# Optimization experiments

Measured on AMD Instinct MI355X. Metric: run time of the kernel, lower is better.

Reference implementation:

```python
import jax, jax.numpy as jnp
import numpy as np

BN_EPS = 1e-5
TAU = 1.0  # gumbel temperature

def setup_inputs() -> dict:
    key = jax.random.key(0)
    ks = jax.random.split(key, 6)
    B, O, F, H, HID = 32, 4096, 256, 8, 128
    x = jax.random.normal(ks[0], (B, O, F), dtype=jnp.float32)
    gumbel_noise = jax.random.gumbel(ks[1], (B, O, H), dtype=jnp.float32)
    W_in = jax.random.normal(ks[2], (F, HID), dtype=jnp.float32) * (1.0 / np.sqrt(F))
    b_in = jnp.zeros((HID,), jnp.float32)
    W_blk = jax.random.normal(ks[3], (HID, HID), dtype=jnp.float32) * (1.0 / np.sqrt(HID))
    b_blk = jnp.zeros((HID,), jnp.float32)
    bn_gamma = jnp.ones((HID,), jnp.float32)
    bn_beta = jnp.zeros((HID,), jnp.float32)
    W_fc = jax.random.normal(ks[4], (HID, H), dtype=jnp.float32) * (1.0 / np.sqrt(HID))
    b_fc = jnp.zeros((H,), jnp.float32)
    return {"x": x, "gumbel_noise": gumbel_noise, "W_in": W_in, "b_in": b_in,
            "W_blk": W_blk, "b_blk": b_blk, "bn_gamma": bn_gamma, "bn_beta": bn_beta,
            "W_fc": W_fc, "b_fc": b_fc}

def reference(x, gumbel_noise, W_in, b_in, W_blk, b_blk, bn_gamma, bn_beta, W_fc, b_fc):
    B, O, F = x.shape
    xf = x.reshape(B * O, F)
    # DynamicNetwork head: input linear + relu, one residual block (Linear+BN+ReLU), fc
    h = jax.nn.relu(xf @ W_in + b_in)  # (B*O, HID)
    z = h @ W_blk + b_blk
    mu = z.mean(axis=0)
    var = z.var(axis=0)  # biased var, matches BatchNorm training normalization
    z = (z - mu) * jax.lax.rsqrt(var + BN_EPS) * bn_gamma + bn_beta
    h = jax.nn.relu(z) + h  # residual
    logits = (h @ W_fc + b_fc).reshape(B, O, -1)  # (B, O, H)
    # mask out zero-norm observations
    mask = (jnp.linalg.norm(x, axis=2) != 0)[..., None].astype(x.dtype)  # (B, O, 1)
    logits = logits * mask
    # gumbel softmax over observation dim (soft)
    w = jax.nn.softmax((logits + gumbel_noise) / TAU, axis=1)  # (B, O, H)
    # weighted sum pooling: algebraically the repeat-multiply-sum in the original
    pooled = jnp.einsum('boh,bof->bhf', w, x)  # (B, H, F)
    return pooled.reshape(B, -1)  # (B, H*F)
```

## Files before the change

### kernel.cpp

```cpp
#include <hip/hip_runtime.h>
#include <hip/hip_bf16.h>
#include <math.h>

#define MB_ 131072
#define F_  256
#define HID_ 128
#define H_  8
#define O_  4096
#define B_  32

typedef __attribute__((ext_vector_type(8))) short short8;
typedef __attribute__((ext_vector_type(4))) float f32x4;

static __device__ __forceinline__ unsigned short f2bf(float f) {
    unsigned int u = __float_as_uint(f);
    unsigned int r = (u + 0x7fffu + ((u >> 16) & 1u)) >> 16;
    return (unsigned short)r;
}
static __device__ __forceinline__ float bf2f(unsigned short u) {
    return __uint_as_float(((unsigned int)u) << 16);
}
static __device__ __forceinline__ unsigned int pk2bf(float a, float b) {
    float2 f2; f2.x = a; f2.y = b;
    __hip_bfloat162 h = __float22bfloat162_rn(f2);
    union { __hip_bfloat162 h2; unsigned int u; } cv;
    cv.h2 = h;
    return cv.u;
}

__global__ __launch_bounds__(256) void k_prep(
    const float* __restrict__ W_in, const float* __restrict__ W_blk,
    unsigned short* __restrict__ Win_f, unsigned short* __restrict__ Wblk_f)
{
    const int idx = blockIdx.x * 256 + threadIdx.x;
    if (idx < 32768) {
        const int j = idx & 7, n = (idx >> 3) & 127, c = idx >> 10;
        Win_f[idx] = f2bf(W_in[(size_t)(c * 8 + j) * HID_ + n]);
    } else if (idx < 49152) {
        const int i2 = idx - 32768;
        const int j = i2 & 7, n = (i2 >> 3) & 127, c = i2 >> 10;
        Wblk_f[i2] = f2bf(W_blk[(size_t)(c * 8 + j) * HID_ + n]);
    }
}

__global__ __launch_bounds__(256, 3) void k_phaseA(
    const float* __restrict__ x, const unsigned short* __restrict__ Win_f,
    const unsigned short* __restrict__ Wblk_f,
    const float* __restrict__ b_in, const float* __restrict__ b_blk,
    unsigned short* __restrict__ h_out, float* __restrict__ mask_out,
    float* __restrict__ sumP, float* __restrict__ sumsqP)
{
    __shared__ __align__(16) unsigned short a_s[2][4 * 132 * 8];
    __shared__ __align__(16) unsigned short hb_s[128 * 136];
    __shared__ float csum_s[128], csumsq_s[128];

    const int tid = threadIdx.x;
    const int R0 = blockIdx.x * 128;
    const int wave = tid >> 6;
    const int wrow = wave >> 1, wcol = wave & 1;
    const int lane = tid & 63;
    const int lm = lane & 15, quad = lane >> 4;
    const int srow = tid >> 3;
    const int sk = tid & 7;
    const int sq = sk >> 1, sh = sk & 1;

    if (tid < 128) { csum_s[tid] = 0.f; csumsq_s[tid] = 0.f; }

    f32x4 acc[4][4];
#pragma unroll
    for (int i = 0; i < 4; i++)
#pragma unroll
        for (int j = 0; j < 4; j++) acc[i][j] = (f32x4){0.f, 0.f, 0.f, 0.f};
    float ms[4] = {0.f, 0.f, 0.f, 0.f};

    const float* xrow = x + (size_t)(R0 + srow) * F_ + sk * 4;

#pragma unroll
    for (int p = 0; p < 4; p++) {
        const float4 v = *(const float4*)(xrow + (size_t)(32 * p) * F_);
        ms[p] += v.x * v.x + v.y * v.y + v.z * v.z + v.w * v.w;
        uint2 w; w.x = pk2bf(v.x, v.y); w.y = pk2bf(v.z, v.w);
        *(uint2*)(&a_s[0][(sq * 132 + srow + 32 * p) * 8 + sh * 4]) = w;
    }
    __syncthreads();

    for (int kt = 0; kt < 8; kt++) {
        const int cur = kt & 1;
        float4 nv[4];
        if (kt < 7) {
#pragma unroll
            for (int p = 0; p < 4; p++)
                nv[p] = *(const float4*)(xrow + (kt + 1) * 32 + (size_t)(32 * p) * F_);
        }
        short8 bfr[4], af[4];
        const unsigned short* wf = Win_f + ((size_t)(kt * 4 + quad) * 128 + wcol * 64 + lm) * 8;
#pragma unroll
        for (int ni = 0; ni < 4; ni++)
            bfr[ni] = *(const short8*)(wf + ni * 16 * 8);
#pragma unroll
        for (int mi = 0; mi < 4; mi++)
            af[mi] = *(const short8*)(&a_s[cur][(quad * 132 + wrow * 64 + mi * 16 + lm) * 8]);
#pragma unroll
        for (int mi = 0; mi < 4; mi++)
#pragma unroll
            for (int ni = 0; ni < 4; ni++)
                acc[mi][ni] = __builtin_amdgcn_mfma_f32_16x16x32_bf16(af[mi], bfr[ni], acc[mi][ni], 0, 0, 0);
        if (kt < 7) {
#pragma unroll
            for (int p = 0; p < 4; p++) {
                ms[p] += nv[p].x * nv[p].x + nv[p].y * nv[p].y
                       + nv[p].z * nv[p].z + nv[p].w * nv[p].w;
                uint2 w; w.x = pk2bf(nv[p].x, nv[p].y); w.y = pk2bf(nv[p].z, nv[p].w);
                *(uint2*)(&a_s[1 - cur][(sq * 132 + srow + 32 * p) * 8 + sh * 4]) = w;
            }
        }
        __syncthreads();
    }

#pragma unroll
    for (int p = 0; p < 4; p++) {
        float s = ms[p];
        s += __shfl_down(s, 4, 8);
        s += __shfl_down(s, 2, 8);
        s += __shfl_down(s, 1, 8);
        if (sk == 0) mask_out[R0 + srow + 32 * p] = (s != 0.f) ? 1.f : 0.f;
    }

    {
        float bcol[4];
#pragma unroll
        for (int ni = 0; ni < 4; ni++) bcol[ni] = b_in[wcol * 64 + ni * 16 + lm];
#pragma unroll
        for (int mi = 0; mi < 4; mi++)
#pragma unroll
            for (int r = 0; r < 4; r++) {
                const int row = wrow * 64 + mi * 16 + quad * 4 + r;
#pragma unroll
                for (int ni = 0; ni < 4; ni++) {
                    const int col = wcol * 64 + ni * 16 + lm;
                    hb_s[row * 136 + col] = f2bf(fmaxf(acc[mi][ni][r] + bcol[ni], 0.f));
                }
            }
    }
    __syncthreads();

    {
        const int row = tid >> 1, half = tid & 1;
#pragma unroll
        for (int c8 = 0; c8 < 8; c8++) {
            const short8 v = *(const short8*)(&hb_s[row * 136 + half * 64 + c8 * 8]);
            *(short8*)(h_out + (size_t)(R0 + row) * HID_ + half * 64 + c8 * 8) = v;
        }
    }

#pragma unroll
    for (int i = 0; i < 4; i++)
#pragma unroll
        for (int j = 0; j < 4; j++) acc[i][j] = (f32x4){0.f, 0.f, 0.f, 0.f};
#pragma unroll
    for (int kt = 0; kt < 4; kt++) {
        short8 af[4], bfr[4];
        const unsigned short* wf2 = Wblk_f + ((size_t)(kt * 4 + quad) * 128 + wcol * 64 + lm) * 8;
#pragma unroll
        for (int ni = 0; ni < 4; ni++)
            bfr[ni] = *(const short8*)(wf2 + ni * 16 * 8);
#pragma unroll
        for (int mi = 0; mi < 4; mi++)
            af[mi] = *(const short8*)(&hb_s[(wrow * 64 + mi * 16 + lm) * 136 + kt * 32 + quad * 8]);
#pragma unroll
        for (int mi = 0; mi < 4; mi++)
#pragma unroll
            for (int ni = 0; ni < 4; ni++)
                acc[mi][ni] = __builtin_amdgcn_mfma_f32_16x16x32_bf16(af[mi], bfr[ni], acc[mi][ni], 0, 0, 0);
    }

    {
        float bcol[4];
#pragma unroll
        for (int ni = 0; ni < 4; ni++) bcol[ni] = b_blk[wcol * 64 + ni * 16 + lm];
        float s_c[4] = {0.f, 0.f, 0.f, 0.f}, ss_c[4] = {0.f, 0.f, 0.f, 0.f};
#pragma unroll
        for (int mi = 0; mi < 4; mi++)
#pragma unroll
            for (int r = 0; r < 4; r++)
#pragma unroll
                for (int ni = 0; ni < 4; ni++) {
                    const float zv = acc[mi][ni][r] + bcol[ni];
                    s_c[ni] += zv;
                    ss_c[ni] += zv * zv;
                }
#pragma unroll
        for (int ni = 0; ni < 4; ni++) {
            float s = s_c[ni], ss = ss_c[ni];
            s  += __shfl_xor(s, 16);  s  += __shfl_xor(s, 32);
            ss += __shfl_xor(ss, 16); ss += __shfl_xor(ss, 32);
            if (quad == 0) {
                atomicAdd(&csum_s[wcol * 64 + ni * 16 + lm], s);
                atomicAdd(&csumsq_s[wcol * 64 + ni * 16 + lm], ss);
            }
        }
    }
    __syncthreads();
    if (tid < 128) {
        sumP[(size_t)blockIdx.x * 128 + tid] = csum_s[tid];
        sumsqP[(size_t)blockIdx.x * 128 + tid] = csumsq_s[tid];
    }
}

__global__ __launch_bounds__(256) void k_bnfin(
    const float* __restrict__ sumP, const float* __restrict__ sumsqP,
    const float* __restrict__ gamma, const float* __restrict__ beta,
    float* __restrict__ scale, float* __restrict__ shift)
{
    const int c = blockIdx.x;
    const int tid = threadIdx.x;
    float s = 0.f, ss = 0.f;
    for (int i = tid; i < 1024; i += 256) {
        s  += sumP[(size_t)i * 128 + c];
        ss += sumsqP[(size_t)i * 128 + c];
    }
#pragma unroll
    for (int off = 32; off; off >>= 1) {
        s  += __shfl_xor(s, off, 64);
        ss += __shfl_xor(ss, off, 64);
    }
    __shared__ float rs[4], rss[4];
    const int wid = tid >> 6, lane = tid & 63;
    if (lane == 0) { rs[wid] = s; rss[wid] = ss; }
    __syncthreads();
    if (tid == 0) {
        const float S  = rs[0] + rs[1] + rs[2] + rs[3];
        const float SS = rss[0] + rss[1] + rss[2] + rss[3];
        const float inv_m = 1.0f / (float)MB_;
        const float mu = S * inv_m;
        const float var = SS * inv_m - mu * mu;
        const float sc = gamma[c] * rsqrtf(var + 1e-5f);
        scale[c] = sc;
        shift[c] = beta[c] - mu * sc;
    }
}

__global__ __launch_bounds__(256, 4) void k_phaseC(
    const unsigned short* __restrict__ h_in, const unsigned short* __restrict__ Wblk_f,
    const float* __restrict__ b_blk,
    const float* __restrict__ scale, const float* __restrict__ shift,
    const float* __restrict__ W_fc, const float* __restrict__ b_fc,
    const float* __restrict__ mask, const float* __restrict__ gumbel,
    float* __restrict__ t_bho)
{
    __shared__ __align__(16) unsigned short hb_s[128 * 136];
    __shared__ float wfc_s[128 * 8];
    __shared__ float sc_s[128], sh_s[128];

    const int tid = threadIdx.x;
    const int R0 = blockIdx.x * 128;
    const int wave = tid >> 6;
    const int wrow = wave >> 1, wcol = wave & 1;
    const int lane = tid & 63;
    const int lm = lane & 15, quad = lane >> 4;

    for (int i = tid; i < 1024; i += 256) wfc_s[i] = W_fc[i];
    if (tid < 128) { sc_s[tid] = scale[tid]; sh_s[tid] = shift[tid]; }
    {
        const int row = tid >> 1, half = tid & 1;
#pragma unroll
        for (int c8 = 0; c8 < 8; c8++) {
            const short8 v = *(const short8*)(h_in + (size_t)(R0 + row) * HID_ + half * 64 + c8 * 8);
            *(short8*)(&hb_s[row * 136 + half * 64 + c8 * 8]) = v;
        }
    }
    __syncthreads();

    f32x4 acc[4][4];
#pragma unroll
    for (int i = 0; i < 4; i++)
#pragma unroll
        for (int j = 0; j < 4; j++) acc[i][j] = (f32x4){0.f, 0.f, 0.f, 0.f};
#pragma unroll
    for (int kt = 0; kt < 4; kt++) {
        short8 af[4], bfr[4];
        const unsigned short* wf2 = Wblk_f + ((size_t)(kt * 4 + quad) * 128 + wcol * 64 + lm) * 8;
#pragma unroll
        for (int ni = 0; ni < 4; ni++)
            bfr[ni] = *(const short8*)(wf2 + ni * 16 * 8);
#pragma unroll
        for (int mi = 0; mi < 4; mi++)
            af[mi] = *(const short8*)(&hb_s[(wrow * 64 + mi * 16 + lm) * 136 + kt * 32 + quad * 8]);
#pragma unroll
        for (int mi = 0; mi < 4; mi++)
#pragma unroll
            for (int ni = 0; ni < 4; ni++)
                acc[mi][ni] = __builtin_amdgcn_mfma_f32_16x16x32_bf16(af[mi], bfr[ni], acc[mi][ni], 0, 0, 0);
    }

    {
        float bcol[4];
#pragma unroll
        for (int ni = 0; ni < 4; ni++) bcol[ni] = b_blk[wcol * 64 + ni * 16 + lm];
#pragma unroll
        for (int mi = 0; mi < 4; mi++)
#pragma unroll
            for (int r = 0; r < 4; r++) {
                const int row = wrow * 64 + mi * 16 + quad * 4 + r;
#pragma unroll
                for (int ni = 0; ni < 4; ni++) {
                    const int col = wcol * 64 + ni * 16 + lm;
                    const float zv = acc[mi][ni][r] + bcol[ni];
                    const float hv = bf2f(hb_s[row * 136 + col]);
                    const float hb = fmaxf(zv * sc_s[col] + sh_s[col], 0.f) + hv;
                    hb_s[row * 136 + col] = f2bf(hb);
                }
            }
    }
    __syncthreads();

    {
        const int row = tid >> 1, half = tid & 1;
        const int grow = R0 + row;
        float a8[8];
#pragma unroll
        for (int j = 0; j < 8; j++) a8[j] = 0.f;
#pragma unroll 2
        for (int k8 = 0; k8 < 8; k8++) {
            const short8 hv8 = *(const short8*)(&hb_s[row * 136 + half * 64 + k8 * 8]);
#pragma unroll
            for (int e = 0; e < 8; e++) {
                const float hv = bf2f((unsigned short)hv8[e]);
                const int k = half * 64 + k8 * 8 + e;
#pragma unroll
                for (int j = 0; j < 8; j++) a8[j] += hv * wfc_s[k * 8 + j];
            }
        }
#pragma unroll
        for (int j = 0; j < 8; j++) a8[j] += __shfl_xor(a8[j], 1);
        const float mk = mask[grow];
        const int b = grow >> 12, o = grow & 4095;
#pragma unroll
        for (int jj = 0; jj < 4; jj++) {
            const int j = half * 4 + jj;
            const float t = (a8[j] + b_fc[j]) * mk + gumbel[(size_t)grow * 8 + j];
            t_bho[((size_t)(b * 8 + j)) * O_ + o] = t;
        }
    }
}

__global__ __launch_bounds__(256) void k_softmax(
    const float* __restrict__ t_in, float* __restrict__ w_out)
{
    const int bh = blockIdx.x;
    const int tid = threadIdx.x;
    const float* tp = t_in + (size_t)bh * O_;
    float4 v[4];
    float mx = -3.4e38f;
#pragma unroll
    for (int it = 0; it < 4; it++) {
        v[it] = *(const float4*)(tp + it * 1024 + tid * 4);
        mx = fmaxf(mx, fmaxf(fmaxf(v[it].x, v[it].y), fmaxf(v[it].z, v[it].w)));
    }
#pragma unroll
    for (int off = 32; off; off >>= 1) mx = fmaxf(mx, __shfl_xor(mx, off, 64));
    __shared__ float rm[4], rsum[4];
    const int wid = tid >> 6, lane = tid & 63;
    if (lane == 0) rm[wid] = mx;
    __syncthreads();
    mx = fmaxf(fmaxf(rm[0], rm[1]), fmaxf(rm[2], rm[3]));
    float sum = 0.f;
#pragma unroll
    for (int it = 0; it < 4; it++) {
        v[it].x = __expf(v[it].x - mx); v[it].y = __expf(v[it].y - mx);
        v[it].z = __expf(v[it].z - mx); v[it].w = __expf(v[it].w - mx);
        sum += v[it].x + v[it].y + v[it].z + v[it].w;
    }
#pragma unroll
    for (int off = 32; off; off >>= 1) sum += __shfl_xor(sum, off, 64);
    if (lane == 0) rsum[wid] = sum;
    __syncthreads();
    sum = rsum[0] + rsum[1] + rsum[2] + rsum[3];
    const float inv = 1.f / sum;
    float* wp = w_out + (size_t)bh * O_;
#pragma unroll
    for (int it = 0; it < 4; it++) {
        float4 o;
        o.x = v[it].x * inv; o.y = v[it].y * inv; o.z = v[it].z * inv; o.w = v[it].w * inv;
        *(float4*)(wp + it * 1024 + tid * 4) = o;
    }
}

__global__ __launch_bounds__(256) void k_pool(
    const float* __restrict__ x, const float* __restrict__ w_in,
    float* __restrict__ pp)
{
    __shared__ float ws_s[8][128];
    const int tid = threadIdx.x;
    const int oc = blockIdx.x;
    const int b = blockIdx.y;
    const int wave = tid >> 6, lane = tid & 63;
    const int f = wave * 64 + lane;
    for (int i = tid; i < 1024; i += 256) {
        const int hh = i >> 7, oi = i & 127;
        ws_s[hh][oi] = w_in[((size_t)(b * 8 + hh)) * O_ + oc * 128 + oi];
    }
    __syncthreads();
    float acc[8];
#pragma unroll
    for (int hh = 0; hh < 8; hh++) acc[hh] = 0.f;
    const float* xp = x + ((size_t)(b * O_ + oc * 128)) * F_ + f;
#pragma unroll 1
    for (int oi = 0; oi < 128; oi += 4) {
        float xv[4];
#pragma unroll
        for (int u = 0; u < 4; u++) xv[u] = xp[(size_t)(oi + u) * F_];
#pragma unroll
        for (int u = 0; u < 4; u++)
#pragma unroll
            for (int hh = 0; hh < 8; hh++) acc[hh] += ws_s[hh][oi + u] * xv[u];
    }
    float* outp = pp + ((size_t)(oc * 32 + b)) * 2048;
#pragma unroll
    for (int hh = 0; hh < 8; hh++) outp[hh * 256 + f] = acc[hh];
}

__global__ __launch_bounds__(256) void k_reduce_pool(
    const float* __restrict__ pp, float* __restrict__ out)
{
    const size_t i = (size_t)blockIdx.x * 256 + threadIdx.x;
    float s = 0.f;
#pragma unroll
    for (int oc = 0; oc < 32; oc++) s += pp[(size_t)oc * 65536 + i];
    out[i] = s;
}

extern "C" void kernel_launch(void* const* d_in, const int* in_sizes, int n_in,
                              void* d_out, int out_size, void* d_ws, size_t ws_size,
                              hipStream_t stream)
{
    const float* x      = (const float*)d_in[0];
    const float* gumbel = (const float*)d_in[1];
    const float* W_in   = (const float*)d_in[2];
    const float* b_in   = (const float*)d_in[3];
    const float* W_blk  = (const float*)d_in[4];
    const float* b_blk  = (const float*)d_in[5];
    const float* gamma  = (const float*)d_in[6];
    const float* beta   = (const float*)d_in[7];
    const float* W_fc   = (const float*)d_in[8];
    const float* b_fc   = (const float*)d_in[9];
    float* out = (float*)d_out;
    char* ws = (char*)d_ws;

    unsigned short* h_bf  = (unsigned short*)(ws + 0);
    float* mask   = (float*)(ws + 33554432);
    float* sumP   = (float*)(ws + 34078720);
    float* sumsqP = (float*)(ws + 34603008);
    float* scale  = (float*)(ws + 35127296);
    float* shift  = (float*)(ws + 35127808);
    float* t_buf  = (float*)(ws + 35128320);
    float* w_buf  = (float*)(ws + 39322624);
    float* pp     = (float*)(ws + 43516928);
    unsigned short* Win_f  = (unsigned short*)(ws + 51905536);
    unsigned short* Wblk_f = (unsigned short*)(ws + 51971072);

    k_prep<<<192, 256, 0, stream>>>(W_in, W_blk, Win_f, Wblk_f);
    k_phaseA<<<1024, 256, 0, stream>>>(x, Win_f, Wblk_f, b_in, b_blk, h_bf, mask, sumP, sumsqP);
    k_bnfin<<<128, 256, 0, stream>>>(sumP, sumsqP, gamma, beta, scale, shift);
    k_phaseC<<<1024, 256, 0, stream>>>(h_bf, Wblk_f, b_blk, scale, shift, W_fc, b_fc, mask, gumbel, t_buf);
    k_softmax<<<256, 256, 0, stream>>>(t_buf, w_buf);
    k_pool<<<dim3(32, 32), 256, 0, stream>>>(x, w_buf, pp);
    k_reduce_pool<<<256, 256, 0, stream>>>(pp, out);
}
```

Before: 331.4 us.

## Split phaseA into gemm1 and gemm2stats kernels with MFMA-fragment h layout

Splits the fused first-GEMM/second-GEMM-stats kernel into two kernels. The first GEMM kernel drops double buffering of x into a single shared buffer, which lowers its LDS use. The h activation is stored in a blocked, MFMA-fragment-friendly layout so the stats kernel can read A fragments straight from global memory and phaseC can load it linearly. This adds an extra kernel launch and a global re-read of h, and it loses the overlap of x loads with MFMA in gemm1.

```diff
diff --git a/kernel.cpp b/kernel.cpp
--- a/kernel.cpp
+++ b/kernel.cpp
@@ -43,16 +43,14 @@
     }
 }
 
-__global__ __launch_bounds__(256, 3) void k_phaseA(
+__global__ __launch_bounds__(256, 3) void k_gemm1(
     const float* __restrict__ x, const unsigned short* __restrict__ Win_f,
-    const unsigned short* __restrict__ Wblk_f,
-    const float* __restrict__ b_in, const float* __restrict__ b_blk,
-    unsigned short* __restrict__ h_out, float* __restrict__ mask_out,
-    float* __restrict__ sumP, float* __restrict__ sumsqP)
-{
-    __shared__ __align__(16) unsigned short a_s[2][4 * 132 * 8];
-    __shared__ __align__(16) unsigned short hb_s[128 * 136];
-    __shared__ float csum_s[128], csumsq_s[128];
+    const float* __restrict__ b_in,
+    unsigned short* __restrict__ h_f, float* __restrict__ mask_out)
+{
+    __shared__ __align__(16) unsigned short smem[128 * 136];
+    unsigned short* a_s = smem;
+    unsigned short* hb_s = smem;
 
     const int tid = threadIdx.x;
     const int R0 = blockIdx.x * 128;
@@ -64,8 +62,6 @@
     const int sk = tid & 7;
     const int sq = sk >> 1, sh = sk & 1;
 
-    if (tid < 128) { csum_s[tid] = 0.f; csumsq_s[tid] = 0.f; }
-
     f32x4 acc[4][4];
 #pragma unroll
     for (int i = 0; i < 4; i++)
@@ -75,45 +71,28 @@
 
     const float* xrow = x + (size_t)(R0 + srow) * F_ + sk * 4;
 
-#pragma unroll
-    for (int p = 0; p < 4; p++) {
-        const float4 v = *(const float4*)(xrow + (size_t)(32 * p) * F_);
-        ms[p] += v.x * v.x + v.y * v.y + v.z * v.z + v.w * v.w;
-        uint2 w; w.x = pk2bf(v.x, v.y); w.y = pk2bf(v.z, v.w);
-        *(uint2*)(&a_s[0][(sq * 132 + srow + 32 * p) * 8 + sh * 4]) = w;
-    }
-    __syncthreads();
-
     for (int kt = 0; kt < 8; kt++) {
-        const int cur = kt & 1;
-        float4 nv[4];
-        if (kt < 7) {
-#pragma unroll
-            for (int p = 0; p < 4; p++)
-                nv[p] = *(const float4*)(xrow + (kt + 1) * 32 + (size_t)(32 * p) * F_);
+#pragma unroll
+        for (int p = 0; p < 4; p++) {
+            const float4 v = *(const float4*)(xrow + kt * 32 + (size_t)(32 * p) * F_);
+            ms[p] += v.x * v.x + v.y * v.y + v.z * v.z + v.w * v.w;
+            uint2 w; w.x = pk2bf(v.x, v.y); w.y = pk2bf(v.z, v.w);
+            *(uint2*)(&a_s[(sq * 132 + srow + 32 * p) * 8 + sh * 4]) = w;
         }
-        short8 bfr[4], af[4];
+        __syncthreads();
+        short8 af[4], bfr[4];
         const unsigned short* wf = Win_f + ((size_t)(kt * 4 + quad) * 128 + wcol * 64 + lm) * 8;
 #pragma unroll
         for (int ni = 0; ni < 4; ni++)
             bfr[ni] = *(const short8*)(wf + ni * 16 * 8);
 #pragma unroll
         for (int mi = 0; mi < 4; mi++)
-            af[mi] = *(const short8*)(&a_s[cur][(quad * 132 + wrow * 64 + mi * 16 + lm) * 8]);
+            af[mi] = *(const short8*)(&a_s[(quad * 132 + wrow * 64 + mi * 16 + lm) * 8]);
 #pragma unroll
         for (int mi = 0; mi < 4; mi++)
 #pragma unroll
             for (int ni = 0; ni < 4; ni++)
                 acc[mi][ni] = __builtin_amdgcn_mfma_f32_16x16x32_bf16(af[mi], bfr[ni], acc[mi][ni], 0, 0, 0);
-        if (kt < 7) {
-#pragma unroll
-            for (int p = 0; p < 4; p++) {
-                ms[p] += nv[p].x * nv[p].x + nv[p].y * nv[p].y
-                       + nv[p].z * nv[p].z + nv[p].w * nv[p].w;
-                uint2 w; w.x = pk2bf(nv[p].x, nv[p].y); w.y = pk2bf(nv[p].z, nv[p].w);
-                *(uint2*)(&a_s[1 - cur][(sq * 132 + srow + 32 * p) * 8 + sh * 4]) = w;
-            }
-        }
         __syncthreads();
     }
 
@@ -144,15 +123,34 @@
     }
     __syncthreads();
 
-    {
-        const int row = tid >> 1, half = tid & 1;
-#pragma unroll
-        for (int c8 = 0; c8 < 8; c8++) {
-            const short8 v = *(const short8*)(&hb_s[row * 136 + half * 64 + c8 * 8]);
-            *(short8*)(h_out + (size_t)(R0 + row) * HID_ + half * 64 + c8 * 8) = v;
-        }
-    }
-
+    unsigned short* hf = h_f + (size_t)blockIdx.x * 16384;
+#pragma unroll
+    for (int i = 0; i < 8; i++) {
+        const int idx = i * 256 + tid;
+        const int c = idx >> 7, row = idx & 127;
+        const short8 v = *(const short8*)(&hb_s[row * 136 + c * 8]);
+        *(short8*)(hf + (size_t)idx * 8) = v;
+    }
+}
+
+__global__ __launch_bounds__(256, 4) void k_gemm2stats(
+    const unsigned short* __restrict__ h_f, const unsigned short* __restrict__ Wblk_f,
+    const float* __restrict__ b_blk,
+    float* __restrict__ sumP, float* __restrict__ sumsqP)
+{
+    __shared__ float csum_s[128], csumsq_s[128];
+    const int tid = threadIdx.x;
+    const int wave = tid >> 6;
+    const int wrow = wave >> 1, wcol = wave & 1;
+    const int lane = tid & 63;
+    const int lm = lane & 15, quad = lane >> 4;
+
+    if (tid < 128) { csum_s[tid] = 0.f; csumsq_s[tid] = 0.f; }
+    __syncthreads();
+
+    const unsigned short* hf = h_f + (size_t)blockIdx.x * 16384;
+
+    f32x4 acc[4][4];
 #pragma unroll
     for (int i = 0; i < 4; i++)
 #pragma unroll
@@ -166,7 +164,7 @@
             bfr[ni] = *(const short8*)(wf2 + ni * 16 * 8);
 #pragma unroll
         for (int mi = 0; mi < 4; mi++)
-            af[mi] = *(const short8*)(&hb_s[(wrow * 64 + mi * 16 + lm) * 136 + kt * 32 + quad * 8]);
+            af[mi] = *(const short8*)(hf + ((size_t)(kt * 4 + quad) * 128 + wrow * 64 + mi * 16 + lm) * 8);
 #pragma unroll
         for (int mi = 0; mi < 4; mi++)
 #pragma unroll
@@ -174,30 +172,28 @@
                 acc[mi][ni] = __builtin_amdgcn_mfma_f32_16x16x32_bf16(af[mi], bfr[ni], acc[mi][ni], 0, 0, 0);
     }
 
-    {
-        float bcol[4];
-#pragma unroll
-        for (int ni = 0; ni < 4; ni++) bcol[ni] = b_blk[wcol * 64 + ni * 16 + lm];
-        float s_c[4] = {0.f, 0.f, 0.f, 0.f}, ss_c[4] = {0.f, 0.f, 0.f, 0.f};
-#pragma unroll
-        for (int mi = 0; mi < 4; mi++)
-#pragma unroll
-            for (int r = 0; r < 4; r++)
-#pragma unroll
-                for (int ni = 0; ni < 4; ni++) {
-                    const float zv = acc[mi][ni][r] + bcol[ni];
-                    s_c[ni] += zv;
-                    ss_c[ni] += zv * zv;
-                }
-#pragma unroll
-        for (int ni = 0; ni < 4; ni++) {
-            float s = s_c[ni], ss = ss_c[ni];
-            s  += __shfl_xor(s, 16);  s  += __shfl_xor(s, 32);
-            ss += __shfl_xor(ss, 16); ss += __shfl_xor(ss, 32);
-            if (quad == 0) {
-                atomicAdd(&csum_s[wcol * 64 + ni * 16 + lm], s);
-                atomicAdd(&csumsq_s[wcol * 64 + ni * 16 + lm], ss);
+    float bcol[4];
+#pragma unroll
+    for (int ni = 0; ni < 4; ni++) bcol[ni] = b_blk[wcol * 64 + ni * 16 + lm];
+    float s_c[4] = {0.f, 0.f, 0.f, 0.f}, ss_c[4] = {0.f, 0.f, 0.f, 0.f};
+#pragma unroll
+    for (int mi = 0; mi < 4; mi++)
+#pragma unroll
+        for (int r = 0; r < 4; r++)
+#pragma unroll
+            for (int ni = 0; ni < 4; ni++) {
+                const float zv = acc[mi][ni][r] + bcol[ni];
+                s_c[ni] += zv;
+                ss_c[ni] += zv * zv;
             }
+#pragma unroll
+    for (int ni = 0; ni < 4; ni++) {
+        float s = s_c[ni], ss = ss_c[ni];
+        s  += __shfl_xor(s, 16);  s  += __shfl_xor(s, 32);
+        ss += __shfl_xor(ss, 16); ss += __shfl_xor(ss, 32);
+        if (quad == 0) {
+            atomicAdd(&csum_s[wcol * 64 + ni * 16 + lm], s);
+            atomicAdd(&csumsq_s[wcol * 64 + ni * 16 + lm], ss);
         }
     }
     __syncthreads();
@@ -240,15 +236,15 @@
     }
 }
 
-__global__ __launch_bounds__(256, 4) void k_phaseC(
-    const unsigned short* __restrict__ h_in, const unsigned short* __restrict__ Wblk_f,
+__global__ __launch_bounds__(256, 3) void k_phaseC(
+    const unsigned short* __restrict__ h_f, const unsigned short* __restrict__ Wblk_f,
     const float* __restrict__ b_blk,
     const float* __restrict__ scale, const float* __restrict__ shift,
     const float* __restrict__ W_fc, const float* __restrict__ b_fc,
     const float* __restrict__ mask, const float* __restrict__ gumbel,
     float* __restrict__ t_bho)
 {
-    __shared__ __align__(16) unsigned short hb_s[128 * 136];
+    __shared__ __align__(16) unsigned short hb_f[16384];
     __shared__ float wfc_s[128 * 8];
     __shared__ float sc_s[128], sh_s[128];
 
@@ -261,13 +257,12 @@
 
     for (int i = tid; i < 1024; i += 256) wfc_s[i] = W_fc[i];
     if (tid < 128) { sc_s[tid] = scale[tid]; sh_s[tid] = shift[tid]; }
-    {
-        const int row = tid >> 1, half = tid & 1;
-#pragma unroll
-        for (int c8 = 0; c8 < 8; c8++) {
-            const short8 v = *(const short8*)(h_in + (size_t)(R0 + row) * HID_ + half * 64 + c8 * 8);
-            *(short8*)(&hb_s[row * 136 + half * 64 + c8 * 8]) = v;
-        }
+    const unsigned short* hf = h_f + (size_t)blockIdx.x * 16384;
+#pragma unroll
+    for (int i = 0; i < 8; i++) {
+        const int idx = i * 256 + tid;
+        const short8 v = *(const short8*)(hf + (size_t)idx * 8);
+        *(short8*)(&hb_f[idx * 8]) = v;
     }
     __syncthreads();
 
@@ -285,13 +280,14 @@
             bfr[ni] = *(const short8*)(wf2 + ni * 16 * 8);
 #pragma unroll
         for (int mi = 0; mi < 4; mi++)
-            af[mi] = *(const short8*)(&hb_s[(wrow * 64 + mi * 16 + lm) * 136 + kt * 32 + quad * 8]);
+            af[mi] = *(const short8*)(&hb_f[((kt * 4 + quad) * 128 + wrow * 64 + mi * 16 + lm) * 8]);
 #pragma unroll
         for (int mi = 0; mi < 4; mi++)
 #pragma unroll
             for (int ni = 0; ni < 4; ni++)
                 acc[mi][ni] = __builtin_amdgcn_mfma_f32_16x16x32_bf16(af[mi], bfr[ni], acc[mi][ni], 0, 0, 0);
     }
+    __syncthreads();
 
     {
         float bcol[4];
@@ -305,10 +301,10 @@
 #pragma unroll
                 for (int ni = 0; ni < 4; ni++) {
                     const int col = wcol * 64 + ni * 16 + lm;
+                    const int a = ((col >> 3) * 128 + row) * 8 + (col & 7);
                     const float zv = acc[mi][ni][r] + bcol[ni];
-                    const float hv = bf2f(hb_s[row * 136 + col]);
-                    const float hb = fmaxf(zv * sc_s[col] + sh_s[col], 0.f) + hv;
-                    hb_s[row * 136 + col] = f2bf(hb);
+                    const float hv = bf2f(hb_f[a]);
+                    hb_f[a] = f2bf(fmaxf(zv * sc_s[col] + sh_s[col], 0.f) + hv);
                 }
             }
     }
@@ -321,12 +317,13 @@
 #pragma unroll
         for (int j = 0; j < 8; j++) a8[j] = 0.f;
 #pragma unroll 2
-        for (int k8 = 0; k8 < 8; k8++) {
-            const short8 hv8 = *(const short8*)(&hb_s[row * 136 + half * 64 + k8 * 8]);
+        for (int c8 = 0; c8 < 8; c8++) {
+            const int c = half * 8 + c8;
+            const short8 hv8 = *(const short8*)(&hb_f[(c * 128 + row) * 8]);
 #pragma unroll
             for (int e = 0; e < 8; e++) {
                 const float hv = bf2f((unsigned short)hv8[e]);
-                const int k = half * 64 + k8 * 8 + e;
+                const int k = c * 8 + e;
 #pragma unroll
                 for (int j = 0; j < 8; j++) a8[j] += hv * wfc_s[k * 8 + j];
             }
@@ -447,7 +444,7 @@
     float* out = (float*)d_out;
     char* ws = (char*)d_ws;
 
-    unsigned short* h_bf  = (unsigned short*)(ws + 0);
+    unsigned short* h_f   = (unsigned short*)(ws + 0);
     float* mask   = (float*)(ws + 33554432);
     float* sumP   = (float*)(ws + 34078720);
     float* sumsqP = (float*)(ws + 34603008);
@@ -460,9 +457,10 @@
     unsigned short* Wblk_f = (unsigned short*)(ws + 51971072);
 
     k_prep<<<192, 256, 0, stream>>>(W_in, W_blk, Win_f, Wblk_f);
-    k_phaseA<<<1024, 256, 0, stream>>>(x, Win_f, Wblk_f, b_in, b_blk, h_bf, mask, sumP, sumsqP);
+    k_gemm1<<<1024, 256, 0, stream>>>(x, Win_f, b_in, h_f, mask);
+    k_gemm2stats<<<1024, 256, 0, stream>>>(h_f, Wblk_f, b_blk, sumP, sumsqP);
     k_bnfin<<<128, 256, 0, stream>>>(sumP, sumsqP, gamma, beta, scale, shift);
-    k_phaseC<<<1024, 256, 0, stream>>>(h_bf, Wblk_f, b_blk, scale, shift, W_fc, b_fc, mask, gumbel, t_buf);
+    k_phaseC<<<1024, 256, 0, stream>>>(h_f, Wblk_f, b_blk, scale, shift, W_fc, b_fc, mask, gumbel, t_buf);
     k_softmax<<<256, 256, 0, stream>>>(t_buf, w_buf);
     k_pool<<<dim3(32, 32), 256, 0, stream>>>(x, w_buf, pp);
     k_reduce_pool<<<256, 256, 0, stream>>>(pp, out);
```

Measured after the change: 316.3 us. 4.5% less time.
